# Optimization experiments

Measured on AMD Instinct MI355X. Metric: run time of the kernel, lower is better.

## Reference

```python
import jax, jax.numpy as jnp
import numpy as np

B, T, D, H = 4, 2048, 1024, 16
DK = D // H

def setup_inputs() -> dict:
    key = jax.random.key(0)
    k1, k2, k3 = jax.random.split(key, 3)
    s = 1.0 / np.sqrt(D)
    return {
        "x": jax.random.normal(k1, (B, T, D), dtype=jnp.float32),
        "W_qkv": jax.random.normal(k2, (D, 3 * D), dtype=jnp.float32) * s,
        "b_qkv": jnp.zeros((3 * D,), dtype=jnp.float32),
        "W_out": jax.random.normal(k3, (D, D), dtype=jnp.float32) * s,
        "b_out": jnp.zeros((D,), dtype=jnp.float32),
    }

def reference(x, W_qkv, b_qkv, W_out, b_out):
    Bx, Tx, C = x.shape
    qkv = x @ W_qkv + b_qkv                       # [B,T,3D]
    q, k, v = jnp.split(qkv, 3, axis=-1)
    # [B,T,D] -> [B,H,T,dk]
    def heads(t):
        return t.reshape(Bx, Tx, H, DK).transpose(0, 2, 1, 3)
    q, k, v = heads(q), heads(k), heads(v)
    scores = jnp.einsum('bhqd,bhkd->bhqk', q, k) / jnp.sqrt(jnp.float32(DK))
    causal = jnp.tril(jnp.ones((Tx, Tx), dtype=bool))  # [T,T]
    scores = jnp.where(causal[None, None], scores, -jnp.inf)
    attn = jax.nn.softmax(scores, axis=-1)        # dropout p=0 (eval)
    out = jnp.einsum('bhqk,bhkd->bhqd', attn, v)  # [B,H,T,dk]
    out = out.transpose(0, 2, 1, 3).reshape(Bx, Tx, C)
    return out @ W_out + b_out
```

## Files before the change

kernel.cpp:

```cpp
#include <hip/hip_runtime.h>
#include <hip/hip_bf16.h>
#include <stdint.h>

#define T_SEQ 2048
#define DMODEL 1024
#define NH 16
#define DKH 64
#define M_TOK 8192
#define N_QKV 3072
#define K_DIM 1024

#define ATTN_SC (0.125f * 1.44269504f)

typedef __attribute__((ext_vector_type(8))) short short8;
typedef __attribute__((ext_vector_type(4))) short short4v;
typedef __attribute__((ext_vector_type(4))) float float4v;
typedef __attribute__((ext_vector_type(2))) unsigned int uint2v;

__device__ inline short bf16_bits(float f) {
  __hip_bfloat16 h = __float2bfloat16(f);
  short s;
  __builtin_memcpy(&s, &h, 2);
  return s;
}

__device__ inline short4v pack4_bf16_fast(float a, float b, float c, float d) {
  unsigned ua = __builtin_bit_cast(unsigned, a) + 0x8000u;
  unsigned ub = __builtin_bit_cast(unsigned, b) + 0x8000u;
  unsigned uc = __builtin_bit_cast(unsigned, c) + 0x8000u;
  unsigned ud = __builtin_bit_cast(unsigned, d) + 0x8000u;
  uint2v uu = {(ua >> 16) | (ub & 0xFFFF0000u),
               (uc >> 16) | (ud & 0xFFFF0000u)};
  return __builtin_bit_cast(short4v, uu);
}

__device__ inline short4v pack4_bf16_trunc(float a, float b, float c, float d) {
  unsigned ua = __builtin_bit_cast(unsigned, a);
  unsigned ub = __builtin_bit_cast(unsigned, b);
  unsigned uc = __builtin_bit_cast(unsigned, c);
  unsigned ud = __builtin_bit_cast(unsigned, d);
  uint2v uu = {__builtin_amdgcn_perm(ub, ua, 0x07060302u),
               __builtin_amdgcn_perm(ud, uc, 0x07060302u)};
  return __builtin_bit_cast(short4v, uu);
}

__device__ inline void async_load16(const void* g, void* l) {
  __builtin_amdgcn_global_load_lds(
      (const __attribute__((address_space(1))) unsigned int*)g,
      (__attribute__((address_space(3))) unsigned int*)l,
      16, 0, 0);
}


__global__ __launch_bounds__(256) void cvt_kernel(const float* __restrict__ in,
                                                  short* __restrict__ out, int n) {
  int idx = (blockIdx.x * 256 + threadIdx.x) * 4;
  if (idx < n) {
    float4v v = *(const float4v*)(in + idx);
    short4v o;
    o[0] = bf16_bits(v[0]); o[1] = bf16_bits(v[1]);
    o[2] = bf16_bits(v[2]); o[3] = bf16_bits(v[3]);
    *(short4v*)(out + idx) = o;
  }
}

__global__ __launch_bounds__(256) void transpose_cvt(const float* __restrict__ in,
                                                     short* __restrict__ out,
                                                     int K, int N) {
  __shared__ float tile[32][33];
  int n0 = blockIdx.x * 32, k0 = blockIdx.y * 32;
  int tx = threadIdx.x, ty = threadIdx.y;
  #pragma unroll
  for (int r = ty; r < 32; r += 8)
    tile[r][tx] = in[(size_t)(k0 + r) * N + n0 + tx];
  __syncthreads();
  #pragma unroll
  for (int r = ty; r < 32; r += 8)
    out[(size_t)(n0 + r) * K + k0 + tx] = bf16_bits(tile[tx][r]);
}


template <int EPI>
__global__ __launch_bounds__(256) void gemm_bt(
    const short* __restrict__ A, const short* __restrict__ Bt,
    const float* __restrict__ bias,
    short* __restrict__ Qb, short* __restrict__ Kf, short* __restrict__ Vf,
    float* __restrict__ Cout, int M, int N, int K, int ntile0) {
  constexpr bool CT = (EPI != 1);
  __shared__ __align__(16) short AsB[2][128 * 32];
  __shared__ __align__(16) short BsB[2][128 * 32];
  const int tid = threadIdx.x;
  const int lane = tid & 63;
  const int wave = tid >> 6;
  const int m0 = blockIdx.x * 128;
  const int n0 = (blockIdx.y + ntile0) * 128;
  const int wm = (wave >> 1) * 64;
  const int wn = (wave & 1) * 64;
  const int quad = lane >> 4;
  const int l16 = lane & 15;

  float4v acc[4][4] = {};

  const int r0 = tid >> 2, r1 = r0 + 64;
  const int oswz = (((tid & 3) - (tid >> 3)) & 3) * 8;
  const int lo0 = wave * 512;
  const int lo1 = 2048 + wave * 512;

  const short* Ag0 = A  + (size_t)(m0 + r0) * K + oswz;
  const short* Ag1 = A  + (size_t)(m0 + r1) * K + oswz;
  const short* Bg0 = Bt + (size_t)(n0 + r0) * K + oswz;
  const short* Bg1 = Bt + (size_t)(n0 + r1) * K + oswz;

  const int sw = ((quad + (l16 >> 1)) & 3) * 8;

  async_load16(Ag0, &AsB[0][0] + lo0);
  async_load16(Ag1, &AsB[0][0] + lo1);
  async_load16(Bg0, &BsB[0][0] + lo0);
  async_load16(Bg1, &BsB[0][0] + lo1);

  const int nkt = K >> 5;
  for (int it = 0; it < nkt; ++it) {
    __builtin_amdgcn_s_waitcnt(0);
    __syncthreads();

    if (it + 1 < nkt) {
      const int kt = (it + 1) << 5;
      const int nb = (it + 1) & 1;
      async_load16(Ag0 + kt, &AsB[nb][0] + lo0);
      async_load16(Ag1 + kt, &AsB[nb][0] + lo1);
      async_load16(Bg0 + kt, &BsB[nb][0] + lo0);
      async_load16(Bg1 + kt, &BsB[nb][0] + lo1);
    }

    const short* As = &AsB[it & 1][0];
    const short* Bs = &BsB[it & 1][0];
    short8 af[4], bfr[4];
    #pragma unroll
    for (int t = 0; t < 4; ++t)
      af[t] = *(const short8*)(As + (size_t)(wm + t * 16 + l16) * 32 + sw);
    #pragma unroll
    for (int t = 0; t < 4; ++t)
      bfr[t] = *(const short8*)(Bs + (size_t)(wn + t * 16 + l16) * 32 + sw);
    #pragma unroll
    for (int i = 0; i < 4; ++i)
      #pragma unroll
      for (int j = 0; j < 4; ++j) {
        if (CT)
          acc[i][j] = __builtin_amdgcn_mfma_f32_16x16x32_bf16(bfr[j], af[i], acc[i][j], 0, 0, 0);
        else
          acc[i][j] = __builtin_amdgcn_mfma_f32_16x16x32_bf16(af[i], bfr[j], acc[i][j], 0, 0, 0);
      }
  }

  if (EPI == 0) {
    const int which = n0 >> 10;
    #pragma unroll
    for (int tj = 0; tj < 4; ++tj) {
      const int colb = n0 + wn + tj * 16 + quad * 4;
      float4v bz = *(const float4v*)(bias + colb);
      const int d = colb & 1023;
      const int h = d >> 6, dkb = d & 63;
      #pragma unroll
      for (int ti = 0; ti < 4; ++ti) {
        const int tok = m0 + wm + ti * 16 + l16;
        const int b = tok >> 11, t = tok & 2047;
        const size_t bhoff = (size_t)(b * NH + h) * (T_SEQ * DKH);
        float4v v = acc[ti][tj];
        if (which == 0) {
          short4v o = pack4_bf16_fast((v[0] + bz[0]) * ATTN_SC, (v[1] + bz[1]) * ATTN_SC,
                                      (v[2] + bz[2]) * ATTN_SC, (v[3] + bz[3]) * ATTN_SC);
          *(short4v*)(Qb + bhoff + (size_t)t * DKH + dkb) = o;
        } else {
          short4v o = pack4_bf16_fast(v[0] + bz[0], v[1] + bz[1], v[2] + bz[2], v[3] + bz[3]);
          const int h2 = dkb >> 5, qd = (dkb >> 3) & 3, w = dkb & 7;
          size_t kbase = bhoff + (size_t)(t >> 6) * 4096 +
                         ((((t >> 4) & 3) * 2 + h2) * 4 + qd) * 128 + (t & 15) * 8 + w;
          *(short4v*)(Kf + kbase) = o;
        }
      }
    }
  } else if (EPI == 1) {
    #pragma unroll
    for (int tj = 0; tj < 4; ++tj) {
      const int col = n0 + wn + tj * 16 + l16;
      const float bz = bias[col];
      const int d = col & 1023;
      const int h = d >> 6, dk = d & 63;
      #pragma unroll
      for (int ti = 0; ti < 4; ++ti) {
        const int rbase = m0 + wm + ti * 16 + quad * 4;
        const int b = rbase >> 11, t = rbase & 2047;
        const size_t bhoff = (size_t)(b * NH + h) * (T_SEQ * DKH);
        float4v v = acc[ti][tj];
        short4v pv = pack4_bf16_fast(v[0] + bz, v[1] + bz, v[2] + bz, v[3] + bz);
        size_t off = bhoff + (size_t)(t >> 6) * 4096 +
                     ((((t >> 4) & 3) * 4 + (dk >> 4)) * 4 + ((t >> 2) & 3)) * 64 +
                     (dk & 15) * 4;
        *(short4v*)(Vf + off) = pv;
      }
    }
  } else {
    #pragma unroll
    for (int tj = 0; tj < 4; ++tj) {
      const int colb = n0 + wn + tj * 16 + quad * 4;
      float4v bz = *(const float4v*)(bias + colb);
      #pragma unroll
      for (int ti = 0; ti < 4; ++ti) {
        const int row = m0 + wm + ti * 16 + l16;
        float4v v = acc[ti][tj];
        float4v o = {v[0] + bz[0], v[1] + bz[1], v[2] + bz[2], v[3] + bz[3]};
        *(float4v*)(Cout + (size_t)row * N + colb) = o;
      }
    }
  }
}


template <int MASK>
__device__ __forceinline__ void attn_tile(
    const short* __restrict__ Ks, const short* __restrict__ Vs,
    const short8 aq[2][2], short4v ones,
    float4v oc[2][4], float4v lc[2],
    int dkq, int quad, int l16) {
  const int mb = dkq + quad * 4 - l16;
  #pragma unroll
  for (int c = 0; c < 4; ++c) {
    short8 b0 = *(const short8*)(Ks + (c * 2 + 0) * 512 + quad * 128 + l16 * 8);
    short8 b1 = *(const short8*)(Ks + (c * 2 + 1) * 512 + quad * 128 + l16 * 8);
    short4v vf[4];
    #pragma unroll
    for (int d = 0; d < 4; ++d)
      vf[d] = *(const short4v*)(Vs + (c * 4 + d) * 256 + quad * 64 + l16 * 4);
    #pragma unroll
    for (int qi = 0; qi < 2; ++qi) {
      float4v z = {0.f, 0.f, 0.f, 0.f};
      z = __builtin_amdgcn_mfma_f32_16x16x32_bf16(b0, aq[qi][0], z, 0, 0, 0);
      z = __builtin_amdgcn_mfma_f32_16x16x32_bf16(b1, aq[qi][1], z, 0, 0, 0);
      float p[4];
      #pragma unroll
      for (int i = 0; i < 4; ++i) {
        p[i] = __builtin_amdgcn_exp2f(z[i]);
        if (MASK && (mb + c * 16 + i - qi * 16 > 0)) p[i] = 0.f;
      }
      short4v pb = pack4_bf16_trunc(p[0], p[1], p[2], p[3]);
      lc[qi] = __builtin_amdgcn_mfma_f32_16x16x16bf16_1k(ones, pb, lc[qi], 0, 0, 0);
      #pragma unroll
      for (int d = 0; d < 4; ++d)
        oc[qi][d] = __builtin_amdgcn_mfma_f32_16x16x16bf16_1k(vf[d], pb, oc[qi][d], 0, 0, 0);
    }
  }
}

__global__ __launch_bounds__(256) void attn_kernel(const short* __restrict__ Qb,
                                                   const short* __restrict__ Kf,
                                                   const short* __restrict__ Vf,
                                                   short* __restrict__ Ao) {
  __shared__ __align__(16) short KsB[2][4096];
  __shared__ __align__(16) short VsB[2][4096];
  const int bh = blockIdx.x;
  const int y = blockIdx.y;
  const int qb = (y < 4) ? (15 - y) : (y < 8) ? (y - 4) : (y < 12) ? (19 - y) : (y - 8);
  const int tid = threadIdx.x;
  const int lane = tid & 63, wave = tid >> 6;
  const int quad = lane >> 4, l16 = lane & 15;
  const int qw0 = qb * 128 + wave * 32;
  const int nkb = 2 * qb + 2;

  const short* Qg = Qb + ((size_t)bh * T_SEQ + qw0) * DKH;
  const short* Kg0 = Kf + (size_t)bh * (T_SEQ * DKH);
  const short* Vg0 = Vf + (size_t)bh * (T_SEQ * DKH);

  short8 aq[2][2];
  #pragma unroll
  for (int qi = 0; qi < 2; ++qi)
    #pragma unroll
    for (int h = 0; h < 2; ++h)
      aq[qi][h] = *(const short8*)(Qg + (size_t)(qi * 16 + l16) * DKH + h * 32 + quad * 8);

  float4v oc[2][4] = {};
  float4v lc[2] = {};
  short4v ones = {0x3F80, 0x3F80, 0x3F80, 0x3F80};

  async_load16(Kg0 + tid * 8,        &KsB[0][0] + wave * 512);
  async_load16(Kg0 + 2048 + tid * 8, &KsB[0][0] + 2048 + wave * 512);
  async_load16(Vg0 + tid * 8,        &VsB[0][0] + wave * 512);
  async_load16(Vg0 + 2048 + tid * 8, &VsB[0][0] + 2048 + wave * 512);

  for (int kb = 0; kb < nkb; ++kb) {
    __builtin_amdgcn_s_waitcnt(0);
    __syncthreads();

    if (kb + 1 < nkb) {
      const int nb = (kb + 1) & 1;
      const short* Kg = Kg0 + (size_t)(kb + 1) * 4096;
      const short* Vg = Vg0 + (size_t)(kb + 1) * 4096;
      async_load16(Kg + tid * 8,        &KsB[nb][0] + wave * 512);
      async_load16(Kg + 2048 + tid * 8, &KsB[nb][0] + 2048 + wave * 512);
      async_load16(Vg + tid * 8,        &VsB[nb][0] + wave * 512);
      async_load16(Vg + 2048 + tid * 8, &VsB[nb][0] + 2048 + wave * 512);
    }

    const int dkq = kb * 64 - qw0;
    if (dkq + 63 <= 0) {
      attn_tile<0>(&KsB[kb & 1][0], &VsB[kb & 1][0], aq, ones, oc, lc, dkq, quad, l16);
    } else if (dkq <= 31) {
      attn_tile<1>(&KsB[kb & 1][0], &VsB[kb & 1][0], aq, ones, oc, lc, dkq, quad, l16);
    }
  }

  const int b = bh >> 4, h = bh & 15;
  #pragma unroll
  for (int qi = 0; qi < 2; ++qi) {
    float rl = 1.0f / lc[qi][0];
    #pragma unroll
    for (int d = 0; d < 4; ++d) {
      short4v o;
      #pragma unroll
      for (int i = 0; i < 4; ++i) o[i] = bf16_bits(oc[qi][d][i] * rl);
      int t = qw0 + qi * 16 + l16;
      *(short4v*)(Ao + (size_t)(b * T_SEQ + t) * DMODEL + h * DKH + d * 16 + quad * 4) = o;
    }
  }
}


extern "C" void kernel_launch(void* const* d_in, const int* in_sizes, int n_in,
                              void* d_out, int out_size, void* d_ws, size_t ws_size,
                              hipStream_t stream) {
  const float* x    = (const float*)d_in[0];
  const float* Wqkv = (const float*)d_in[1];
  const float* bqkv = (const float*)d_in[2];
  const float* Wout = (const float*)d_in[3];
  const float* bout = (const float*)d_in[4];
  float* out = (float*)d_out;

  char* ws = (char*)d_ws;
  short* Xb    = (short*)(ws);
  short* Wqkvt = (short*)(ws + (16ull << 20));
  short* Woutt = (short*)(ws + (22ull << 20));
  short* Qb    = (short*)(ws + (24ull << 20));
  short* Kf    = (short*)(ws + (40ull << 20));
  short* Vf    = (short*)(ws + (56ull << 20));
  short* Ao    = (short*)(ws + (72ull << 20));

  cvt_kernel<<<(M_TOK * K_DIM / 4 + 255) / 256, 256, 0, stream>>>(x, Xb, M_TOK * K_DIM);
  dim3 tb(32, 8);
  transpose_cvt<<<dim3(N_QKV / 32, K_DIM / 32), tb, 0, stream>>>(Wqkv, Wqkvt, K_DIM, N_QKV);
  transpose_cvt<<<dim3(DMODEL / 32, K_DIM / 32), tb, 0, stream>>>(Wout, Woutt, K_DIM, DMODEL);

  gemm_bt<0><<<dim3(M_TOK / 128, 16), 256, 0, stream>>>(
      Xb, Wqkvt, bqkv, Qb, Kf, nullptr, nullptr, M_TOK, N_QKV, K_DIM, 0);
  gemm_bt<1><<<dim3(M_TOK / 128, 8), 256, 0, stream>>>(
      Xb, Wqkvt, bqkv, nullptr, nullptr, Vf, nullptr, M_TOK, N_QKV, K_DIM, 16);

  attn_kernel<<<dim3(64, T_SEQ / 128), 256, 0, stream>>>(Qb, Kf, Vf, Ao);

  gemm_bt<2><<<dim3(M_TOK / 128, DMODEL / 128), 256, 0, stream>>>(
      Ao, Woutt, bout, nullptr, nullptr, nullptr, out, M_TOK, DMODEL, K_DIM, 0);
}
```

Baseline: 243.2 us.

## Triple-buffer GEMM shared-memory tiles with partial vmcnt waits

```diff
diff --git a/kernel.cpp b/kernel.cpp
--- a/kernel.cpp
+++ b/kernel.cpp
@@ -87,8 +87,8 @@
     short* __restrict__ Qb, short* __restrict__ Kf, short* __restrict__ Vf,
     float* __restrict__ Cout, int M, int N, int K, int ntile0) {
   constexpr bool CT = (EPI != 1);
-  __shared__ __align__(16) short AsB[2][128 * 32];
-  __shared__ __align__(16) short BsB[2][128 * 32];
+  __shared__ __align__(16) short AsB[3][128 * 32];
+  __shared__ __align__(16) short BsB[3][128 * 32];
   const int tid = threadIdx.x;
   const int lane = tid & 63;
   const int wave = tid >> 6;
@@ -113,27 +113,30 @@
 
   const int sw = ((quad + (l16 >> 1)) & 3) * 8;
 
-  async_load16(Ag0, &AsB[0][0] + lo0);
-  async_load16(Ag1, &AsB[0][0] + lo1);
-  async_load16(Bg0, &BsB[0][0] + lo0);
-  async_load16(Bg1, &BsB[0][0] + lo1);
+  auto stage = [&](int t, int b) {
+    const int kt = t << 5;
+    async_load16(Ag0 + kt, &AsB[b][0] + lo0);
+    async_load16(Ag1 + kt, &AsB[b][0] + lo1);
+    async_load16(Bg0 + kt, &BsB[b][0] + lo0);
+    async_load16(Bg1 + kt, &BsB[b][0] + lo1);
+  };
 
   const int nkt = K >> 5;
+  stage(0, 0);
+  stage(1, 1);
+
+  int c0 = 0, c1 = 1, c2 = 2;
   for (int it = 0; it < nkt; ++it) {
-    __builtin_amdgcn_s_waitcnt(0);
-    __syncthreads();
-
-    if (it + 1 < nkt) {
-      const int kt = (it + 1) << 5;
-      const int nb = (it + 1) & 1;
-      async_load16(Ag0 + kt, &AsB[nb][0] + lo0);
-      async_load16(Ag1 + kt, &AsB[nb][0] + lo1);
-      async_load16(Bg0 + kt, &BsB[nb][0] + lo0);
-      async_load16(Bg1 + kt, &BsB[nb][0] + lo1);
-    }
-
-    const short* As = &AsB[it & 1][0];
-    const short* Bs = &BsB[it & 1][0];
+    if (it < nkt - 1)
+      __builtin_amdgcn_s_waitcnt(0x0F74);
+    else
+      __builtin_amdgcn_s_waitcnt(0x0F70);
+    __builtin_amdgcn_s_barrier();
+    __builtin_amdgcn_sched_barrier(0);
+    if (it + 2 < nkt) stage(it + 2, c2);
+
+    const short* As = &AsB[c0][0];
+    const short* Bs = &BsB[c0][0];
     short8 af[4], bfr[4];
     #pragma unroll
     for (int t = 0; t < 4; ++t)
@@ -150,6 +153,8 @@
         else
           acc[i][j] = __builtin_amdgcn_mfma_f32_16x16x32_bf16(af[i], bfr[j], acc[i][j], 0, 0, 0);
       }
+
+    const int tr = c0; c0 = c1; c1 = c2; c2 = tr;
   }
 
   if (EPI == 0) {
```

Result: slower. 254.5 us (+4.6%).
